# Performance work log

Measured on AMD Instinct MI355X. Metric: run time of the kernel, lower is better.

The kernel has to match this reference:

```python
import jax, jax.numpy as jnp
import numpy as np

B, N, QN, C, H = 4, 1024, 512, 1024, 16
D = C // H  # head_dim = 64


def setup_inputs() -> dict:
    key = jax.random.key(0)
    ks = jax.random.split(key, 8)
    w = lambda k, shape: jax.random.normal(k, shape, jnp.float32) * 0.02
    return dict(
        x=jax.random.normal(ks[0], (B, N, C), jnp.float32),
        query=jax.random.normal(ks[1], (B, QN, C), jnp.float32),
        w_qkv=w(ks[2], (3 * C, C)),        # self.qkv (no bias)
        w_kv=w(ks[3], (2 * C, C)),         # self.to_query_kv (no bias)
        w_qlin=w(ks[4], (3 * C, C)),       # self.query_linear (no bias)
        gate=jnp.zeros((1, H, 1, 1), jnp.float32),  # zero-initialized gate param
        w_proj=w(ks[5], (C, C)),
        b_proj=jnp.zeros((C,), jnp.float32),
        w_qproj=w(ks[6], (C, C)),
        b_qproj=jnp.zeros((C,), jnp.float32),
    )


def _sdpa(q, k, v, scale):
    # q,k,v: [B,H,S,D]; standard softmax attention (attn_mask=None, p=0)
    s = jnp.einsum('bhqd,bhkd->bhqk', q, k) * scale
    return jnp.einsum('bhqk,bhkd->bhqd', jax.nn.softmax(s, axis=-1), v)


def reference(x, query, w_qkv, w_kv, w_qlin, gate, w_proj, b_proj, w_qproj, b_qproj):
    scale = 1.0 / np.sqrt(D)
    # qkv on x -> [3,B,H,N,D]
    qkv = (x @ w_qkv.T).reshape(B, N, 3, H, D).transpose(2, 0, 3, 1, 4)
    q, k, v = qkv[0], qkv[1], qkv[2]
    # kv for cross path computed from ORIGINAL x (before self-attn), as in torch code
    kv = (x @ w_kv.T).reshape(B, N, 2, H, D).transpose(2, 0, 3, 1, 4)
    xk0, xv0 = kv[0], kv[1]
    # self-attention on x (x_mask=None)
    x_attn = _sdpa(q, k, v, scale)  # [B,H,N,D]
    # query qkv -> [3,B,H,QN,D]
    qq3 = (query @ w_qlin.T).reshape(B, QN, 3, H, D).transpose(2, 0, 3, 1, 4)
    qq, qk, qv = qq3[0], qq3[1], qq3[2]
    xk = jnp.concatenate([xk0, qk], axis=2)  # [B,H,N+QN,D]
    xv = jnp.concatenate([xv0, qv], axis=2)
    scores = jnp.einsum('bhqd,bhkd->bhqk', qq, xk) * scale  # [B,H,QN,N+QN]
    # split softmax with tanh-gated first segment (mask=None; dropout p=0)
    gated = jnp.concatenate(
        [jnp.tanh(gate) * jax.nn.softmax(scores[..., :N], axis=-1),
         jax.nn.softmax(scores[..., N:], axis=-1)], axis=-1)
    q_attn = jnp.einsum('bhqk,bhkd->bhqd', gated, xv)  # [B,H,QN,D]
    x_out = x_attn.transpose(0, 2, 1, 3).reshape(B, N, C) @ w_proj.T + b_proj
    q_out = q_attn.transpose(0, 2, 1, 3).reshape(B, QN, C) @ w_qproj.T + b_qproj
    return (x_out, q_out)
```

## Files before the change

kernel.cpp:

```cpp
#include <hip/hip_runtime.h>


using bf16 = __bf16;
typedef __bf16 bf16x4 __attribute__((ext_vector_type(4)));
typedef __bf16 bf16x8 __attribute__((ext_vector_type(8)));
typedef float  f32x4  __attribute__((ext_vector_type(4)));
typedef float  f32x16 __attribute__((ext_vector_type(16)));
typedef unsigned int u32x4 __attribute__((ext_vector_type(4)));

#define MFMA16(a, b, c) __builtin_amdgcn_mfma_f32_16x16x32_bf16((a), (b), (c), 0, 0, 0)
#define MFMA32(a, b, c) __builtin_amdgcn_mfma_f32_32x32x16_bf16((a), (b), (c), 0, 0, 0)

__device__ __forceinline__ int swz128(int row) { return ((row ^ (row >> 3)) & 7) << 4; }

__device__ __forceinline__ void gl_lds16(const void* g, void* l) {
  __builtin_amdgcn_global_load_lds(
      (const __attribute__((address_space(1))) unsigned int*)g,
      (__attribute__((address_space(3))) unsigned int*)l, 16, 0, 0);
}

__device__ __forceinline__ unsigned pack2(float a, float b) {
  unsigned short ua = __builtin_bit_cast(unsigned short, (bf16)a);
  unsigned short ub = __builtin_bit_cast(unsigned short, (bf16)b);
  return (unsigned)ua | ((unsigned)ub << 16);
}

__device__ __forceinline__ float exp2_fast(float x) {
  float r;
  asm("v_exp_f32 %0, %1" : "=v"(r) : "v"(x));
  return r;
}

#define WAITV(N) asm volatile("s_waitcnt vmcnt(" #N ")" ::: "memory")
#define LGKM0()  asm volatile("s_waitcnt lgkmcnt(0)" ::: "memory")
#define SCHED0() __builtin_amdgcn_sched_barrier(0)
#define RAW_BAR() do { __builtin_amdgcn_s_barrier(); asm volatile("" ::: "memory"); } while (0)

__global__ void k_cast_all(const float* __restrict__ s0, const float* __restrict__ s1,
                           const float* __restrict__ s2, const float* __restrict__ s3,
                           const float* __restrict__ s4, const float* __restrict__ s5,
                           const float* __restrict__ s6, bf16* __restrict__ dst) {
  constexpr size_t MM = 1u << 20;
  constexpr size_t o1 = 4 * MM, o2 = 6 * MM, o3 = 9 * MM, o4 = 11 * MM,
                   o5 = 14 * MM, o6 = 15 * MM, total = 16 * MM;
  size_t stride = (size_t)gridDim.x * blockDim.x * 8;
  for (size_t i = ((size_t)blockIdx.x * blockDim.x + threadIdx.x) * 8; i < total; i += stride) {
    const float* s; size_t loc;
    if (i < o1)      { s = s0; loc = i; }
    else if (i < o2) { s = s1; loc = i - o1; }
    else if (i < o3) { s = s2; loc = i - o2; }
    else if (i < o4) { s = s3; loc = i - o3; }
    else if (i < o5) { s = s4; loc = i - o4; }
    else if (i < o6) { s = s5; loc = i - o5; }
    else             { s = s6; loc = i - o6; }
    float4 a = *(const float4*)(s + loc);
    float4 b = *(const float4*)(s + loc + 4);
    bf16x8 o;
    o[0] = (bf16)a.x; o[1] = (bf16)a.y; o[2] = (bf16)a.z; o[3] = (bf16)a.w;
    o[4] = (bf16)b.x; o[5] = (bf16)b.y; o[6] = (bf16)b.z; o[7] = (bf16)b.w;
    *(bf16x8*)(dst + i) = o;
  }
}

__global__ __launch_bounds__(512)
void k_gemm_big(const bf16* __restrict__ xb, const bf16* __restrict__ qb,
                const bf16* __restrict__ wqkvb, const bf16* __restrict__ wqlinb,
                bf16* __restrict__ XK, bf16* __restrict__ VTs, bf16* __restrict__ VT0,
                bf16* __restrict__ QQK, bf16* __restrict__ VTq) {
  constexpr int K = 1024, NT = 16;
  __shared__ bf16 As[2 * 2 * 256 * 32];
  __shared__ bf16 Bs[2 * 2 * 256 * 32];
  const int tid = threadIdx.x;
  const int lane = tid & 63, w = tid >> 6;
  const int wm = w >> 2, wn = w & 3;
  const int r0 = lane & 15, kg = lane >> 4;
  const int bid = ((int)blockIdx.x & 7) * 52 + ((int)blockIdx.x >> 3);
  int grp, tm, tn;
  const bf16 *Ap, *Bp;
  if (bid < 320) { grp = 0; tm = (bid / 20) * 256; tn = (bid % 20) * 256; Ap = xb; Bp = wqkvb; }
  else { grp = 1; int t = bid - 320; tm = (t / 12) * 256; tn = (t % 12) * 256; Ap = qb; Bp = wqlinb; }

  auto stage = [&](int T, int mat, int kh) {
    const bf16* src = mat ? Bp : Ap;
    const int t0 = mat ? tn : tm;
    char* base = (char*)(mat ? (void*)Bs : (void*)As) + (((T & 1) * 2 + kh) << 14);
#pragma unroll
    for (int i = 0; i < 2; i++) {
      int c = i * 512 + tid;
      int row = c >> 2, g = c & 3;
      int sg = (g ^ ((row >> 1) & 3)) * 8;
      gl_lds16(src + (size_t)(t0 + row) * K + T * 64 + kh * 32 + sg, base + c * 16);
    }
  };
  auto ldA = [&](int bi, int kh, int row) -> bf16x8 {
    return *(const bf16x8*)((const char*)As + ((bi * 2 + kh) << 14) + row * 64 +
                            ((kg ^ ((row >> 1) & 3)) << 4));
  };
  auto ldB = [&](int bi, int kh, int row) -> bf16x8 {
    return *(const bf16x8*)((const char*)Bs + ((bi * 2 + kh) << 14) + row * 64 +
                            ((kg ^ ((row >> 1) & 3)) << 4));
  };

  f32x4 acc[8][4] = {};

  stage(0, 0, 0); stage(0, 1, 0); stage(0, 0, 1); stage(0, 1, 1);
  stage(1, 0, 0); stage(1, 1, 0);
  WAITV(4);
  RAW_BAR();

  for (int j = 0; j < NT; ++j) {
    const int bi = j & 1;
    bf16x8 af[4], bfk[4];
#pragma unroll
    for (int i = 0; i < 4; i++) af[i] = ldA(bi, 0, wm * 128 + i * 16 + r0);
#pragma unroll
    for (int nf = 0; nf < 4; nf++) bfk[nf] = ldB(bi, 0, wn * 64 + nf * 16 + r0);
    if (j + 1 < NT) stage(j + 1, 0, 1);
    RAW_BAR(); LGKM0(); SCHED0();
    __builtin_amdgcn_s_setprio(1);
#pragma unroll
    for (int i = 0; i < 4; i++)
#pragma unroll
      for (int nf = 0; nf < 4; nf++) acc[i][nf] = MFMA16(af[i], bfk[nf], acc[i][nf]);
    __builtin_amdgcn_s_setprio(0);
    RAW_BAR();
#pragma unroll
    for (int i = 0; i < 4; i++) af[i] = ldA(bi, 0, wm * 128 + 64 + i * 16 + r0);
    if (j + 1 < NT) stage(j + 1, 1, 1);
    RAW_BAR(); LGKM0(); SCHED0();
    __builtin_amdgcn_s_setprio(1);
#pragma unroll
    for (int i = 0; i < 4; i++)
#pragma unroll
      for (int nf = 0; nf < 4; nf++) acc[4 + i][nf] = MFMA16(af[i], bfk[nf], acc[4 + i][nf]);
    __builtin_amdgcn_s_setprio(0);
    RAW_BAR();
#pragma unroll
    for (int i = 0; i < 4; i++) af[i] = ldA(bi, 1, wm * 128 + i * 16 + r0);
#pragma unroll
    for (int nf = 0; nf < 4; nf++) bfk[nf] = ldB(bi, 1, wn * 64 + nf * 16 + r0);
    if (j + 2 < NT) stage(j + 2, 0, 0);
    RAW_BAR(); LGKM0(); SCHED0();
    __builtin_amdgcn_s_setprio(1);
#pragma unroll
    for (int i = 0; i < 4; i++)
#pragma unroll
      for (int nf = 0; nf < 4; nf++) acc[i][nf] = MFMA16(af[i], bfk[nf], acc[i][nf]);
    __builtin_amdgcn_s_setprio(0);
    RAW_BAR();
#pragma unroll
    for (int i = 0; i < 4; i++) af[i] = ldA(bi, 1, wm * 128 + 64 + i * 16 + r0);
    if (j + 2 < NT) stage(j + 2, 1, 0);
    RAW_BAR(); LGKM0(); SCHED0();
    __builtin_amdgcn_s_setprio(1);
#pragma unroll
    for (int i = 0; i < 4; i++)
#pragma unroll
      for (int nf = 0; nf < 4; nf++) acc[4 + i][nf] = MFMA16(af[i], bfk[nf], acc[4 + i][nf]);
    __builtin_amdgcn_s_setprio(0);
    if (j < NT - 2) { WAITV(4); } else { WAITV(0); }
    RAW_BAR();
  }

#pragma unroll
  for (int mf = 0; mf < 8; mf++) {
    const int rowb = tm + wm * 128 + mf * 16 + kg * 4;
#pragma unroll
    for (int nf = 0; nf < 4; nf++) {
      const int coln = tn + wn * 64 + nf * 16 + r0;
      bool rm; int rmcol = coln, vbase = 0, tokb = 10, rs_ = 3072;
      bf16* vt = VTs;
      bf16* rmp = XK;
      if (grp == 0) {
        if (tn < 2048)      { rm = true; }
        else if (tn < 3072) { rm = false; vbase = 2048; vt = VTs; }
        else if (tn < 4096) { rm = true; rmcol = coln - 1024; }
        else                { rm = false; vbase = 4096; vt = VT0; }
      } else {
        rs_ = 2048; tokb = 9; rmp = QQK;
        if (tn < 2048) { rm = true; }
        else           { rm = false; vbase = 2048; vt = VTq; }
      }
      if (rm) {
#pragma unroll
        for (int j = 0; j < 4; j++)
          rmp[(size_t)(rowb + j) * rs_ + rmcol] = (bf16)acc[mf][nf][j];
      } else {
        int dg = coln - vbase, h_ = dg >> 6, dd = dg & 63;
        int bq = rowb >> tokb, tok = rowb & ((1 << tokb) - 1);
        bf16x4 wv;
#pragma unroll
        for (int j = 0; j < 4; j++) wv[j] = (bf16)acc[mf][nf][j];
        *(bf16x4*)(vt + (((size_t)((bq * 16 + h_) * 64 + dd)) << tokb) + tok) = wv;
      }
    }
  }
}

__global__ __launch_bounds__(256)
void k_gemm_proj(const bf16* __restrict__ A, const bf16* __restrict__ B0,
                 const bf16* __restrict__ B1, const float* __restrict__ bias0,
                 const float* __restrict__ bias1, float* __restrict__ OUT) {
  constexpr int K = 1024, N = 1024;
  __shared__ bf16 As[128 * 64];
  __shared__ bf16 Bs[128 * 64];
  const int tid = threadIdx.x;
  const int lane = tid & 63, w = tid >> 6;
  const int wr = w >> 1, wc = w & 1;
  const int nbx = N / 128;
  const int bid = ((int)blockIdx.x & 7) * ((int)gridDim.x >> 3) + ((int)blockIdx.x >> 3);
  const int tm = (bid / nbx) * 128, tn = (bid % nbx) * 128;
  const int r0 = lane & 15, kg = lane >> 4;
  const bf16* Bp = (tm < 4096) ? B0 : B1;
  const float* bias = (tm < 4096) ? bias0 : bias1;
  f32x4 acc[4][4] = {};
  for (int kk = 0; kk < K; kk += 64) {
#pragma unroll
    for (int i = 0; i < 4; i++) {
      int c = i * 256 + tid;
      int row = c >> 3, kb = c & 7;
      int sb = (kb ^ ((row ^ (row >> 3)) & 7)) * 8;
      gl_lds16(A + (size_t)(tm + row) * K + kk + sb, (char*)As + c * 16);
      gl_lds16(Bp + (size_t)(tn + row) * K + kk + sb, (char*)Bs + c * 16);
    }
    __syncthreads();
#pragma unroll
    for (int ks = 0; ks < 2; ks++) {
      bf16x8 af[4], bfv[4];
#pragma unroll
      for (int f = 0; f < 4; f++) {
        int rowa = wr * 64 + f * 16 + r0;
        af[f] = *(const bf16x8*)((const char*)As +
                                 ((rowa * 128 + ks * 64 + kg * 16) ^ swz128(rowa)));
        int rowb = wc * 64 + f * 16 + r0;
        bfv[f] = *(const bf16x8*)((const char*)Bs +
                                  ((rowb * 128 + ks * 64 + kg * 16) ^ swz128(rowb)));
      }
#pragma unroll
      for (int mf = 0; mf < 4; mf++)
#pragma unroll
        for (int nf = 0; nf < 4; nf++)
          acc[mf][nf] = MFMA16(af[mf], bfv[nf], acc[mf][nf]);
    }
    __syncthreads();
  }
#pragma unroll
  for (int mf = 0; mf < 4; mf++)
#pragma unroll
    for (int j = 0; j < 4; j++) {
      int row = tm + wr * 64 + mf * 16 + kg * 4 + j;
#pragma unroll
      for (int nf = 0; nf < 4; nf++) {
        int col = tn + wc * 64 + nf * 16 + r0;
        OUT[(size_t)row * 1024 + col] = acc[mf][nf][j] + bias[col];
      }
    }
}

template<int NT>
__device__ __forceinline__ void attn_pass32(
    const bf16* __restrict__ Kg, int kRS,
    const bf16* __restrict__ VTg, int vRS,
    int ntiles, const bf16x8* qf, bf16* Ks, bf16* Vt,
    f32x16* o, float& m, float& rs) {
  const int tid = threadIdx.x;
  const int lane = tid & 63;
  const int lq = lane & 31, kg2 = lane >> 5;

  auto stage = [&](int t) {
    bf16* kd = Ks + (t % 3) * 4096;
    bf16* vd = Vt + (t % 3) * 4096;
    const bf16* kt = Kg + (size_t)t * 64 * kRS;
#pragma unroll
    for (int i = 0; i < 512 / NT; i++) {
      int c = i * NT + tid;
      int r = c >> 3, kb = c & 7;
      int sb = (kb ^ ((r ^ (r >> 3)) & 7)) * 8;
      gl_lds16(kt + (size_t)r * kRS + sb, (char*)kd + c * 16);
    }
#pragma unroll
    for (int i = 0; i < 512 / NT; i++) {
      int c = i * NT + tid;
      int r = c >> 3, kb = c & 7;
      int sb = (kb ^ ((r ^ (r >> 3)) & 7)) * 8;
      gl_lds16(VTg + (size_t)r * vRS + t * 64 + sb, (char*)vd + c * 16);
    }
  };

  stage(0);
  stage(1);
  WAITV(4);
  RAW_BAR();

  for (int t = 0; t < ntiles; t++) {
    const char* KsC = (const char*)(Ks + (t % 3) * 4096);
    const char* VtC = (const char*)(Vt + (t % 3) * 4096);
    const bool more = (t + 2 < ntiles);
    if (more) stage(t + 2);

    f32x16 s[2];
    s[0] = (f32x16)0.f; s[1] = (f32x16)0.f;
    __builtin_amdgcn_s_setprio(1);
#pragma unroll
    for (int kb = 0; kb < 2; kb++) {
      int row = kb * 32 + lq;
#pragma unroll
      for (int dw = 0; dw < 4; dw++) {
        bf16x8 kf = *(const bf16x8*)(KsC + ((row * 128 + dw * 32 + kg2 * 16) ^ swz128(row)));
        s[kb] = MFMA32(kf, qf[dw], s[kb]);
      }
    }
    __builtin_amdgcn_s_setprio(0);

    float vmax = s[0][0];
#pragma unroll
    for (int j = 1; j < 16; j++) vmax = fmaxf(vmax, s[0][j]);
#pragma unroll
    for (int j = 0; j < 16; j++) vmax = fmaxf(vmax, s[1][j]);
    vmax = fmaxf(vmax, __shfl_xor(vmax, 32, 64));
    if (__any(vmax > m + 11.5f)) {
      float mn = fmaxf(m, vmax);
      float fac = exp2_fast(m - mn);
      m = mn;
      rs *= fac;
#pragma unroll
      for (int j = 0; j < 16; j++) {
        int rowq = (j & 3) + 8 * (j >> 2) + 4 * kg2;
        float fj = __shfl(fac, rowq, 64);
        o[0][j] *= fj;
        o[1][j] *= fj;
      }
    }
    float tsum = 0.f;
    f32x16 p[2];
#pragma unroll
    for (int kb = 0; kb < 2; kb++)
#pragma unroll
      for (int j = 0; j < 16; j++) {
        float pv = exp2_fast(s[kb][j] - m);
        p[kb][j] = pv;
        tsum += pv;
      }
    tsum += __shfl_xor(tsum, 32, 64);
    rs += tsum;

    unsigned pk[2][4][2];
#pragma unroll
    for (int kb = 0; kb < 2; kb++)
#pragma unroll
      for (int n = 0; n < 4; n++) {
        pk[kb][n][0] = pack2(p[kb][4 * n + 0], p[kb][4 * n + 1]);
        pk[kb][n][1] = pack2(p[kb][4 * n + 2], p[kb][4 * n + 3]);
      }

#pragma unroll
    for (int w = 0; w < 4; w++) {
      const int kb = w >> 1, wb = w & 1;
      unsigned pushA = kg2 ? pk[kb][2 * wb][0] : pk[kb][2 * wb + 1][0];
      unsigned pushB = kg2 ? pk[kb][2 * wb][1] : pk[kb][2 * wb + 1][1];
      unsigned rcvA = __shfl_xor(pushA, 32, 64);
      unsigned rcvB = __shfl_xor(pushB, 32, 64);
      u32x4 fu;
      fu[0] = kg2 ? rcvA : pk[kb][2 * wb][0];
      fu[1] = kg2 ? rcvB : pk[kb][2 * wb][1];
      fu[2] = kg2 ? pk[kb][2 * wb + 1][0] : rcvA;
      fu[3] = kg2 ? pk[kb][2 * wb + 1][1] : rcvB;
      bf16x8 pfrag = __builtin_bit_cast(bf16x8, fu);
      __builtin_amdgcn_s_setprio(1);
#pragma unroll
      for (int db = 0; db < 2; db++) {
        int d = db * 32 + lq;
        bf16x8 vf = *(const bf16x8*)(VtC + ((d * 128 + w * 32 + kg2 * 16) ^ swz128(d)));
        o[db] = MFMA32(pfrag, vf, o[db]);
      }
      __builtin_amdgcn_s_setprio(0);
    }

    if (more) { WAITV(4); } else { WAITV(0); }
    RAW_BAR();
  }
}

__global__ __launch_bounds__(256)
void k_attn(const bf16* __restrict__ XK, const bf16* __restrict__ QQK,
            const bf16* __restrict__ VTs, const bf16* __restrict__ VT0,
            const bf16* __restrict__ VTq, const float* __restrict__ gate,
            bf16* __restrict__ xat, bf16* __restrict__ qat) {
  __shared__ bf16 Ks[3 * 4096], Vt[3 * 4096];
  const int pb = blockIdx.x;
  const int bid = (pb & 7) * 96 + (pb >> 3);
  const int bh = bid / 12, r = bid % 12;
  const int b = bh >> 4, h = bh & 15;
  const int tid = threadIdx.x, lane = tid & 63, wv = tid >> 6;
  const int lq = lane & 31, kg2 = lane >> 5;
  constexpr float QS = 0.125f * 1.44269504088896f;

  if (r < 8) {
    const int qtok = b * 1024 + r * 128 + wv * 32;
    bf16x8 qf[4];
#pragma unroll
    for (int dw = 0; dw < 4; dw++) {
      qf[dw] = *(const bf16x8*)(XK + (size_t)(qtok + lq) * 3072 + h * 64 + dw * 16 + kg2 * 8);
#pragma unroll
      for (int e = 0; e < 8; e++) qf[dw][e] = (bf16)((float)qf[dw][e] * QS);
    }
    f32x16 o[2];
    o[0] = (f32x16)0.f; o[1] = (f32x16)0.f;
    float m = -__builtin_inff(), rs = 0.f;
    attn_pass32<256>(XK + (size_t)(b * 1024) * 3072 + 1024 + h * 64, 3072,
                     VTs + (size_t)bh * 64 * 1024, 1024,
                     16, qf, Ks, Vt, o, m, rs);
#pragma unroll
    for (int j = 0; j < 16; j++) {
      int rowq = (j & 3) + 8 * (j >> 2) + 4 * kg2;
      float rsj = __shfl(rs, rowq, 64);
      size_t base = (size_t)(qtok + rowq) * 1024 + h * 64;
      xat[base + lq] = (bf16)(o[0][j] / rsj);
      xat[base + 32 + lq] = (bf16)(o[1][j] / rsj);
    }
  } else {
    const int qt = r - 8;
    const int qtok = b * 512 + qt * 128 + wv * 32;
    bf16x8 qf[4];
#pragma unroll
    for (int dw = 0; dw < 4; dw++) {
      qf[dw] = *(const bf16x8*)(QQK + (size_t)(qtok + lq) * 2048 + h * 64 + dw * 16 + kg2 * 8);
#pragma unroll
      for (int e = 0; e < 8; e++) qf[dw][e] = (bf16)((float)qf[dw][e] * QS);
    }
    const float g = tanhf(gate[h]);
    unsigned pka[2][8] = {};
    f32x16 o[2];
    o[0] = (f32x16)0.f; o[1] = (f32x16)0.f;
    float m, rs;
    if (g != 0.0f) {
      m = -__builtin_inff(); rs = 0.f;
      attn_pass32<256>(XK + (size_t)(b * 1024) * 3072 + 2048 + h * 64, 3072,
                       VT0 + (size_t)bh * 64 * 1024, 1024,
                       16, qf, Ks, Vt, o, m, rs);
#pragma unroll
      for (int j2 = 0; j2 < 8; j2++) {
        int j0 = 2 * j2;
        int rq0 = (j0 & 3) + 8 * (j0 >> 2) + 4 * kg2;
        float ra = __shfl(rs, rq0, 64);
        float rb = __shfl(rs, rq0 + 1, 64);
        pka[0][j2] = pack2(g * o[0][j0] / ra, g * o[0][j0 + 1] / rb);
        pka[1][j2] = pack2(g * o[1][j0] / ra, g * o[1][j0 + 1] / rb);
      }
      o[0] = (f32x16)0.f; o[1] = (f32x16)0.f;
    }
    m = -__builtin_inff(); rs = 0.f;
    attn_pass32<256>(QQK + (size_t)(b * 512) * 2048 + 1024 + h * 64, 2048,
                     VTq + (size_t)bh * 64 * 512, 512,
                     8, qf, Ks, Vt, o, m, rs);
#pragma unroll
    for (int j = 0; j < 16; j++) {
      int rowq = (j & 3) + 8 * (j >> 2) + 4 * kg2;
      float rsj = __shfl(rs, rowq, 64);
      size_t base = (size_t)(qtok + rowq) * 1024 + h * 64;
      unsigned wa = pka[0][j >> 1], wb = pka[1][j >> 1];
      unsigned short ua = (j & 1) ? (unsigned short)(wa >> 16) : (unsigned short)(wa & 0xffffu);
      unsigned short ub = (j & 1) ? (unsigned short)(wb >> 16) : (unsigned short)(wb & 0xffffu);
      float a0 = (float)__builtin_bit_cast(bf16, ua);
      float a1 = (float)__builtin_bit_cast(bf16, ub);
      qat[base + lq] = (bf16)(o[0][j] / rsj + a0);
      qat[base + 32 + lq] = (bf16)(o[1][j] / rsj + a1);
    }
  }
}

extern "C" void kernel_launch(void* const* d_in, const int* in_sizes, int n_in,
                              void* d_out, int out_size, void* d_ws, size_t ws_size,
                              hipStream_t stream) {
  (void)in_sizes; (void)n_in; (void)out_size; (void)ws_size;
  const float* x       = (const float*)d_in[0];
  const float* query   = (const float*)d_in[1];
  const float* w_qkv   = (const float*)d_in[2];
  const float* w_kv    = (const float*)d_in[3];
  const float* w_qlin  = (const float*)d_in[4];
  const float* gate    = (const float*)d_in[5];
  const float* w_proj  = (const float*)d_in[6];
  const float* b_proj  = (const float*)d_in[7];
  const float* w_qproj = (const float*)d_in[8];
  const float* b_qproj = (const float*)d_in[9];
  float* out = (float*)d_out;

  bf16* p = (bf16*)d_ws;
  bf16* xb = p;      p += (size_t)4096 * 1024;
  bf16* qb = p;      p += (size_t)2048 * 1024;
  bf16* wqkvb = p;   p += (size_t)3072 * 1024;
  bf16* wkvb = p;    p += (size_t)2048 * 1024;
  bf16* wqlinb = p;  p += (size_t)3072 * 1024;
  bf16* wprojb = p;  p += (size_t)1024 * 1024;
  bf16* wqprojb = p; p += (size_t)1024 * 1024;
  bf16* XK = p;      p += (size_t)4096 * 3072;
  bf16* VTs = p;     p += (size_t)64 * 64 * 1024;
  bf16* VT0 = p;     p += (size_t)64 * 64 * 1024;
  bf16* QQK = p;     p += (size_t)2048 * 2048;
  bf16* VTq = p;     p += (size_t)64 * 64 * 512;
  bf16* xat = p;     p += (size_t)4096 * 1024;
  bf16* qat = p;     p += (size_t)2048 * 1024;
  (void)wkvb;

  k_cast_all<<<2048, 256, 0, stream>>>(x, query, w_qkv, w_kv, w_qlin, w_proj, w_qproj,
                                       (bf16*)d_ws);

  k_gemm_big<<<dim3(416), 512, 0, stream>>>(xb, qb, wqkvb, wqlinb,
                                            XK, VTs, VT0, QQK, VTq);

  k_attn<<<dim3(768), 256, 0, stream>>>(XK, QQK, VTs, VT0, VTq, gate, xat, qat);

  k_gemm_proj<<<dim3(48 * 8), 256, 0, stream>>>(xat, wprojb, wqprojb, b_proj, b_qproj, out);
}
```

Baseline: 179.6 us.

## Switch attention K/V staging to double buffering and regroup block-to-work mapping

The attention inner loop moves from a 3-stage LDS ring with prefetch distance two to a 2-buffer scheme that prefetches only the next tile and waits for all loads each iteration. This cuts LDS use per block (48KB down to 32KB) and may allow more resident blocks, at the cost of less load/compute overlap. The max reduction and exp-sum are rewritten as trees with multiple accumulators to shorten dependency chains, and the probabilities overwrite the score registers. The block index mapping is reorganised so all self-attention blocks come first, followed by all cross-attention blocks.

```diff
diff --git a/kernel.cpp b/kernel.cpp
--- a/kernel.cpp
+++ b/kernel.cpp
@@ -268,8 +268,8 @@
   const int lq = lane & 31, kg2 = lane >> 5;
 
   auto stage = [&](int t) {
-    bf16* kd = Ks + (t % 3) * 4096;
-    bf16* vd = Vt + (t % 3) * 4096;
+    bf16* kd = Ks + (t & 1) * 4096;
+    bf16* vd = Vt + (t & 1) * 4096;
     const bf16* kt = Kg + (size_t)t * 64 * kRS;
 #pragma unroll
     for (int i = 0; i < 512 / NT; i++) {
@@ -288,15 +288,13 @@
   };
 
   stage(0);
-  stage(1);
-  WAITV(4);
+  WAITV(0);
   RAW_BAR();
 
   for (int t = 0; t < ntiles; t++) {
-    const char* KsC = (const char*)(Ks + (t % 3) * 4096);
-    const char* VtC = (const char*)(Vt + (t % 3) * 4096);
-    const bool more = (t + 2 < ntiles);
-    if (more) stage(t + 2);
+    const char* KsC = (const char*)(Ks + (t & 1) * 4096);
+    const char* VtC = (const char*)(Vt + (t & 1) * 4096);
+    if (t + 1 < ntiles) stage(t + 1);
 
     f32x16 s[2];
     s[0] = (f32x16)0.f; s[1] = (f32x16)0.f;
@@ -312,11 +310,13 @@
     }
     __builtin_amdgcn_s_setprio(0);
 
-    float vmax = s[0][0];
-#pragma unroll
-    for (int j = 1; j < 16; j++) vmax = fmaxf(vmax, s[0][j]);
-#pragma unroll
-    for (int j = 0; j < 16; j++) vmax = fmaxf(vmax, s[1][j]);
+    float mm[8];
+#pragma unroll
+    for (int j = 0; j < 8; j++)
+      mm[j] = fmaxf(fmaxf(s[0][j], s[0][j + 8]), fmaxf(s[1][j], s[1][j + 8]));
+    float a0 = fmaxf(mm[0], mm[1]), a1 = fmaxf(mm[2], mm[3]);
+    float a2 = fmaxf(mm[4], mm[5]), a3 = fmaxf(mm[6], mm[7]);
+    float vmax = fmaxf(fmaxf(a0, a1), fmaxf(a2, a3));
     vmax = fmaxf(vmax, __shfl_xor(vmax, 32, 64));
     if (__any(vmax > m + 11.5f)) {
       float mn = fmaxf(m, vmax);
@@ -331,16 +331,19 @@
         o[1][j] *= fj;
       }
     }
-    float tsum = 0.f;
-    f32x16 p[2];
+    float t0 = 0.f, t1 = 0.f, t2 = 0.f, t3 = 0.f;
 #pragma unroll
     for (int kb = 0; kb < 2; kb++)
 #pragma unroll
-      for (int j = 0; j < 16; j++) {
-        float pv = exp2_fast(s[kb][j] - m);
-        p[kb][j] = pv;
-        tsum += pv;
-      }
+      for (int j = 0; j < 16; j += 4) {
+        float p0 = exp2_fast(s[kb][j + 0] - m);
+        float p1 = exp2_fast(s[kb][j + 1] - m);
+        float p2 = exp2_fast(s[kb][j + 2] - m);
+        float p3 = exp2_fast(s[kb][j + 3] - m);
+        s[kb][j + 0] = p0; s[kb][j + 1] = p1; s[kb][j + 2] = p2; s[kb][j + 3] = p3;
+        t0 += p0; t1 += p1; t2 += p2; t3 += p3;
+      }
+    float tsum = (t0 + t1) + (t2 + t3);
     tsum += __shfl_xor(tsum, 32, 64);
     rs += tsum;
 
@@ -349,8 +352,8 @@
     for (int kb = 0; kb < 2; kb++)
 #pragma unroll
       for (int n = 0; n < 4; n++) {
-        pk[kb][n][0] = pack2(p[kb][4 * n + 0], p[kb][4 * n + 1]);
-        pk[kb][n][1] = pack2(p[kb][4 * n + 2], p[kb][4 * n + 3]);
+        pk[kb][n][0] = pack2(s[kb][4 * n + 0], s[kb][4 * n + 1]);
+        pk[kb][n][1] = pack2(s[kb][4 * n + 2], s[kb][4 * n + 3]);
       }
 
 #pragma unroll
@@ -376,7 +379,7 @@
       __builtin_amdgcn_s_setprio(0);
     }
 
-    if (more) { WAITV(4); } else { WAITV(0); }
+    WAITV(0);
     RAW_BAR();
   }
 }
@@ -386,16 +389,16 @@
             const bf16* __restrict__ VTs, const bf16* __restrict__ VT0,
             const bf16* __restrict__ VTq, const float* __restrict__ gate,
             bf16* __restrict__ xat, bf16* __restrict__ qat) {
-  __shared__ bf16 Ks[3 * 4096], Vt[3 * 4096];
+  __shared__ bf16 Ks[2 * 4096], Vt[2 * 4096];
   const int pb = blockIdx.x;
   const int bid = (pb & 7) * 96 + (pb >> 3);
-  const int bh = bid / 12, r = bid % 12;
-  const int b = bh >> 4, h = bh & 15;
   const int tid = threadIdx.x, lane = tid & 63, wv = tid >> 6;
   const int lq = lane & 31, kg2 = lane >> 5;
   constexpr float QS = 0.125f * 1.44269504088896f;
 
-  if (r < 8) {
+  if (bid < 512) {
+    const int bh = bid >> 3, r = bid & 7;
+    const int b = bh >> 4, h = bh & 15;
     const int qtok = b * 1024 + r * 128 + wv * 32;
     bf16x8 qf[4];
 #pragma unroll
@@ -419,7 +422,9 @@
       xat[base + 32 + lq] = (bf16)(o[1][j] / rsj);
     }
   } else {
-    const int qt = r - 8;
+    const int c = bid - 512;
+    const int bh = c >> 2, qt = c & 3;
+    const int b = bh >> 4, h = bh & 15;
     const int qtok = b * 512 + qt * 128 + wv * 32;
     bf16x8 qf[4];
 #pragma unroll
```

Result: no change. 178.3 us (-0.7%).
